# Performance work log

Measured on AMD Instinct MI355X. Metric: run time of the kernel, lower is better.

## Reference

```python
import jax, jax.numpy as jnp
import numpy as np

B, S, D, H, DFF = 2, 2048, 768, 12, 3072
DK = D // H
EPS = 1e-6
NEG = -1e9


def setup_inputs() -> dict:
    key = jax.random.key(0)
    ks = jax.random.split(key, 16)
    s = 1.0 / np.sqrt(D)
    inp = {
        'x': jax.random.normal(ks[0], (B, S, D), jnp.float32),
        'wq': jax.random.normal(ks[1], (D, D), jnp.float32) * s,
        'bq': jnp.zeros((D,), jnp.float32),
        'wk': jax.random.normal(ks[2], (D, D), jnp.float32) * s,
        'bk': jnp.zeros((D,), jnp.float32),
        'wv': jax.random.normal(ks[3], (D, D), jnp.float32) * s,
        'bv': jnp.zeros((D,), jnp.float32),
        'wo': jax.random.normal(ks[4], (D, D), jnp.float32) * s,
        'bo': jnp.zeros((D,), jnp.float32),
        'w1': jax.random.normal(ks[5], (D, DFF), jnp.float32) * s,
        'b1': jnp.zeros((DFF,), jnp.float32),
        'w2': jax.random.normal(ks[6], (DFF, D), jnp.float32) * (1.0 / np.sqrt(DFF)),
        'b2': jnp.zeros((D,), jnp.float32),
        'alpha1': jnp.ones((1,), jnp.float32),
        'beta1': jnp.zeros((1,), jnp.float32),
        'alpha2': jnp.ones((1,), jnp.float32),
        'beta2': jnp.zeros((1,), jnp.float32),
        'mask': jax.random.randint(ks[7], (1, 1, S, S), 0, 2, jnp.int32),
    }
    return inp


def layernorm(x, alpha, beta):
    # torch: mean and UNBIASED std (ddof=1), eps added to std (not variance)
    mean = jnp.mean(x, axis=-1, keepdims=True)
    std = jnp.std(x, axis=-1, keepdims=True, ddof=1)
    return alpha * (x - mean) / (std + EPS) + beta


def encoder_layer(x, wq, bq, wk, bk, wv, bv, wo, bo, w1, b1, w2, b2,
                  alpha1, beta1, alpha2, beta2, mask):
    # projections -> [B, H, S, DK]
    def split_heads(t):
        return t.reshape(B, S, H, DK).transpose(0, 2, 1, 3)
    q = split_heads(x @ wq + bq)
    k = split_heads(x @ wk + bk)
    v = split_heads(x @ wv + bv)
    scores = jnp.einsum('bhqd,bhkd->bhqk', q, k) / np.sqrt(DK)  # [B,H,S,S]
    scores = jnp.where(mask == 0, NEG, scores)
    attn = jax.nn.softmax(scores, axis=-1)
    ctx = jnp.einsum('bhqk,bhkd->bhqd', attn, v)
    ctx = ctx.transpose(0, 2, 1, 3).reshape(B, S, D)
    attn_out = ctx @ wo + bo
    x = layernorm(x + attn_out, alpha1, beta1)
    ff = jax.nn.relu(x @ w1 + b1) @ w2 + b2
    x = layernorm(x + ff, alpha2, beta2)
    return x


def reference(x, wq, bq, wk, bk, wv, bv, wo, bo, w1, b1, w2, b2,
              alpha1, beta1, alpha2, beta2, mask):
    return encoder_layer(x, wq, bq, wk, bk, wv, bv, wo, bo, w1, b1, w2, b2,
                         alpha1, beta1, alpha2, beta2, mask)
```

## Files before the change

### kernel.cpp

```cpp
#include <hip/hip_runtime.h>
#include <hip/hip_bf16.h>


typedef short short8 __attribute__((ext_vector_type(8)));
typedef float floatx4 __attribute__((ext_vector_type(4)));
typedef unsigned short ushort_t;
typedef ushort_t ushort4_t __attribute__((ext_vector_type(4)));

#define B_ 2
#define S_ 2048
#define D_ 768
#define H_ 12
#define DK_ 64
#define DFF_ 3072
#define M_ (B_ * S_)
#define RS_ (3 * D_)

#define LOG2E 1.44269504f
#define FMAX_SHIFT 16.0f

__device__ __forceinline__ float bf2f(ushort_t h) {
  union { unsigned int u; float f; } v; v.u = ((unsigned int)h) << 16; return v.f;
}
__device__ __forceinline__ ushort_t f2bf(float f) {
  union { float f; unsigned int u; } v; v.f = f;
  unsigned int u = v.u;
  unsigned int r = (u + 0x7fffu + ((u >> 16) & 1u)) >> 16;
  return (ushort_t)r;
}

__global__ __launch_bounds__(256) void prep_all(
    const float* __restrict__ wq, const float* __restrict__ wk,
    const float* __restrict__ wv, const float* __restrict__ wo,
    const float* __restrict__ w1, const float* __restrict__ w2,
    ushort_t* __restrict__ wTqkv, ushort_t* __restrict__ woT,
    ushort_t* __restrict__ w1T, ushort_t* __restrict__ w2T,
    const int* __restrict__ mask, ushort_t* __restrict__ maskp,
    const float* __restrict__ x, ushort_t* __restrict__ xb,
    const float* __restrict__ bq, const float* __restrict__ bk,
    const float* __restrict__ bv, float* __restrict__ bqkv) {
  __shared__ ushort_t t[32][33];
  const int blk = blockIdx.x, tid = threadIdx.x;
  if (blk < 6912) {
    const float* in; ushort_t* out; int K, N, bx, by;
    if (blk < 2304) {
      const int z = blk / 576, rr = blk % 576;
      in = (z == 0) ? wq : (z == 1) ? wk : (z == 2) ? wv : wo;
      out = (z < 3) ? (wTqkv + (size_t)z * D_ * D_) : woT;
      K = D_; N = D_; bx = rr % 24; by = rr / 24;
    } else if (blk < 4608) {
      const int rr = blk - 2304;
      in = w1; out = w1T; K = D_; N = DFF_; bx = rr % 96; by = rr / 96;
    } else {
      const int rr = blk - 4608;
      in = w2; out = w2T; K = DFF_; N = D_; bx = rr % 24; by = rr / 24;
    }
    const int nt = bx * 32, kt = by * 32;
    const int tx = tid & 31, ty = tid >> 5;
#pragma unroll
    for (int i = 0; i < 4; i++)
      t[ty + i * 8][tx] = f2bf(in[(size_t)(kt + ty + i * 8) * N + nt + tx]);
    __syncthreads();
#pragma unroll
    for (int i = 0; i < 4; i++)
      out[(size_t)(nt + ty + i * 8) * K + kt + tx] = t[tx][ty + i * 8];
  } else if (blk < 8960) {
    const int tt = (blk - 6912) * 256 + tid;
    const int q = tt >> 8;
    const int cc = tt & 255;
    const int k0 = (cc >> 3) * 64;
    const int g = cc & 7, f = g >> 2, lq = g & 3;
    const int* mrow = mask + (size_t)q * S_ + k0;
    const ushort_t cm = f2bf(-1.4427e9f);
    const ushort_t cu = f2bf(-FMAX_SHIFT * LOG2E);
    short8 o;
#pragma unroll
    for (int n2 = 0; n2 < 2; n2++)
#pragma unroll
      for (int r = 0; r < 4; r++) {
        const int kpl = 32 * f + 16 * n2 + 4 * lq + r;
        o[n2 * 4 + r] = (short)((mrow[kpl] == 0) ? cm : cu);
      }
    *(short8*)(maskp + (size_t)q * S_ + k0 + g * 8) = o;
  } else if (blk < 12032) {
    const int i = ((blk - 8960) * 256 + tid) * 4;
#pragma unroll
    for (int j = 0; j < 4; j++) xb[i + j] = f2bf(x[i + j]);
  } else {
    const int i = (blk - 12032) * 256 + tid;
    if (i < 3 * D_)
      bqkv[i] = (i < D_) ? bq[i] : (i < 2 * D_ ? bk[i - D_] : bv[i - 2 * D_]);
  }
}

template <int BN, int Z, bool VOUT>
__global__ __launch_bounds__(256) void gemm_bt_t(
    const ushort_t* __restrict__ A, const ushort_t* __restrict__ Bt,
    const float* __restrict__ bias, void* __restrict__ Cv,
    ushort_t* __restrict__ vtout,
    int M, int N, int K, int relu, int qcols, float qscale) {
  constexpr int WN = (BN == 128) ? 2 : 1;
  constexpr int WM = 4 / WN;
  constexpr int FI = 128 / WM / 16;
  constexpr int FJ = BN / WN / 16;
  constexpr bool SPLIT = (Z > 1);
  __shared__ __align__(16) ushort_t Al[2][128 * 32];
  __shared__ __align__(16) ushort_t Bl[2][BN * 32];
  const int tid = threadIdx.x;
  const int w = tid >> 6, lane = tid & 63;
  const int wm = (WN == 2) ? (w >> 1) : w;
  const int wn = (WN == 2) ? (w & 1) : 0;
  const int lq = lane >> 4, lr = lane & 15;

  const int NT_n = N / BN;
  const int mg = M >> 10;
  const int lin = blockIdx.x;
  const int xcd = lin & 7, idx = lin >> 3;
  const int m_t = xcd * mg + idx / (NT_n * Z);
  const int rem = idx % (NT_n * Z);
  const int n_t = rem % NT_n;
  const int z   = rem / NT_n;
  const int m0 = m_t * 128, n0 = n_t * BN;

  int kBeg = 0, kEnd = K;
  if (SPLIT) { const int part = K / Z; kBeg = z * part; kEnd = kBeg + part; }
  const int NT = (kEnd - kBeg) / 32;

  auto stage = [&](int kt, int s) {
    const int k0 = kBeg + kt * 32;
#pragma unroll
    for (int i = 0; i < 2; i++) {
      const int base = (w * 2 + i) * 512;
      const int e = base + lane * 8;
      const int row = e >> 5, col = e & 31;
      __builtin_amdgcn_global_load_lds(
          (const __attribute__((address_space(1))) void*)(A + (size_t)(m0 + row) * K + k0 + col),
          (__attribute__((address_space(3))) void*)(&Al[s][base]), 16, 0, 0);
    }
#pragma unroll
    for (int i = 0; i < BN / 64; i++) {
      const int base = (w * (BN / 64) + i) * 512;
      const int e = base + lane * 8;
      const int row = e >> 5, col = e & 31;
      __builtin_amdgcn_global_load_lds(
          (const __attribute__((address_space(1))) void*)(Bt + (size_t)(n0 + row) * K + k0 + col),
          (__attribute__((address_space(3))) void*)(&Bl[s][base]), 16, 0, 0);
    }
  };

  floatx4 acc[FI][FJ];
#pragma unroll
  for (int i = 0; i < FI; i++)
#pragma unroll
    for (int j = 0; j < FJ; j++) acc[i][j] = (floatx4){0.f, 0.f, 0.f, 0.f};

  stage(0, 0);
  for (int kt = 0; kt < NT; kt++) {
    const int s = kt & 1;
    __syncthreads();
    if (kt + 1 < NT) stage(kt + 1, s ^ 1);

    short8 af[FI], bf[FJ];
#pragma unroll
    for (int i = 0; i < FI; i++)
      af[i] = *(const short8*)&Al[s][(wm * (FI * 16) + i * 16 + lr) * 32 + lq * 8];
#pragma unroll
    for (int j = 0; j < FJ; j++)
      bf[j] = *(const short8*)&Bl[s][(wn * (FJ * 16) + j * 16 + lr) * 32 + lq * 8];
#pragma unroll
    for (int i = 0; i < FI; i++)
#pragma unroll
      for (int j = 0; j < FJ; j++)
        acc[i][j] = __builtin_amdgcn_mfma_f32_16x16x32_bf16(af[i], bf[j], acc[i][j], 0, 0, 0);
  }

#pragma unroll
  for (int i = 0; i < FI; i++) {
    const int m = m0 + wm * (FI * 16) + i * 16 + lq * 4;
#pragma unroll
    for (int j = 0; j < FJ; j++) {
      const int n = n0 + wn * (FJ * 16) + j * 16 + lr;
      if (SPLIT) {
        ushort_t* P = (ushort_t*)Cv + (size_t)z * M * N;
#pragma unroll
        for (int r = 0; r < 4; r++)
          P[(size_t)(m + r) * N + n] = f2bf(acc[i][j][r]);
      } else if (VOUT && n >= 2 * D_) {
        const int h = (n - 2 * D_) >> 6, d = (n - 2 * D_) & 63;
        const int bh = (m >> 11) * H_ + h;
        const int kp = m & (S_ - 1);
        const int kw = kp & 63;
        const int pos = (kp & ~63) + ((kw >> 5) << 5) + (((kw >> 2) & 3) << 3)
                      + (((kw >> 4) & 1) << 2);
        const float bv = bias[n];
        ushort4_t o;
#pragma unroll
        for (int r = 0; r < 4; r++) o[r] = f2bf(acc[i][j][r] + bv);
        *(ushort4_t*)(vtout + ((size_t)bh * DK_ + d) * S_ + pos) = o;
      } else {
        const float bv = bias[n];
#pragma unroll
        for (int r = 0; r < 4; r++) {
          float v = acc[i][j][r] + bv;
          if (n < qcols) v *= qscale;
          if (relu) v = v > 0.f ? v : 0.f;
          ((ushort_t*)Cv)[(size_t)(m + r) * N + n] = f2bf(v);
        }
      }
    }
  }
}

__global__ __launch_bounds__(256, 3) void flash_attn(
    const ushort_t* __restrict__ qkv, const ushort_t* __restrict__ vt,
    const ushort_t* __restrict__ maskp, ushort_t* __restrict__ ctx) {
  __shared__ __align__(16) ushort_t lds[2][2][64 * 64];
  const int tid = threadIdx.x;
  const int w = tid >> 6, lane = tid & 63;
  const int wq = w >> 1, wk = w & 1;
  const int lq = lane >> 4, lr = lane & 15;
  const int blk = blockIdx.x;
  const int bh = blk % (B_ * H_), qb = blk / (B_ * H_);
  const int b = bh / H_, h = bh % H_;
  const int q0 = qb * 64;
  const ushort_t* qbase = qkv + (size_t)(b * S_) * RS_ + h * DK_;
  const ushort_t* kbase = qbase + D_;
  const ushort_t* vtb   = vt + (size_t)bh * DK_ * S_;
  const ushort_t* mrow = maskp + (size_t)(q0 + wq * 32 + lr) * S_ + (4 * wk + lq) * 8;

  short8 qfr[2][2];
#pragma unroll
  for (int qf = 0; qf < 2; qf++)
#pragma unroll
    for (int f = 0; f < 2; f++)
      qfr[qf][f] = *(const short8*)(
          qbase + (size_t)(q0 + wq * 32 + qf * 16 + lr) * RS_ + f * 32 + lq * 8);

  auto stage = [&](int k0, int s) {
#pragma unroll
    for (int i = 0; i < 2; i++) {
      const int id = i * 256 + tid;
      const int row = id >> 3;
      const int cc = ((id & 7) ^ (row & 7)) * 8;
      const int dbase = (i * 256 + w * 64) * 8;
      __builtin_amdgcn_global_load_lds(
          (const __attribute__((address_space(1))) void*)(kbase + (size_t)(k0 + row) * RS_ + cc),
          (__attribute__((address_space(3))) void*)(&lds[s][0][dbase]), 16, 0, 0);
      __builtin_amdgcn_global_load_lds(
          (const __attribute__((address_space(1))) void*)(vtb + (size_t)row * S_ + k0 + cc),
          (__attribute__((address_space(3))) void*)(&lds[s][1][dbase]), 16, 0, 0);
    }
  };

  floatx4 oacc[2][4], oli[2];
#pragma unroll
  for (int qf = 0; qf < 2; qf++) {
    oli[qf] = (floatx4){0.f, 0.f, 0.f, 0.f};
#pragma unroll
    for (int dt = 0; dt < 4; dt++) oacc[qf][dt] = (floatx4){0.f, 0.f, 0.f, 0.f};
  }
  short8 ones;
#pragma unroll
  for (int j = 0; j < 8; j++) ones[j] = (short)0x3F80;

  short8 bb[2], bbn[2];
#pragma unroll
  for (int qf = 0; qf < 2; qf++)
    bb[qf] = *(const short8*)(mrow + (size_t)qf * 16 * S_);

  stage(0, 0);
  __syncthreads();

  const int sw8 = lr & 7;
  const int c0 = (lq ^ sw8) * 8;
  const int c1 = ((4 + lq) ^ sw8) * 8;
  const int cW = ((4 * wk + lq) ^ sw8) * 8;

  constexpr int NT = S_ / 64;
  for (int t = 0; t < NT; t++) {
    const int s = t & 1;
    if (t + 1 < NT) {
      stage((t + 1) * 64, s ^ 1);
#pragma unroll
      for (int qf = 0; qf < 2; qf++)
        bbn[qf] = *(const short8*)(mrow + (size_t)qf * 16 * S_ + (t + 1) * 64);
    }

    const ushort_t* kl = &lds[s][0][0];
    const ushort_t* vl = &lds[s][1][0];

    floatx4 sacc[2][2];
#pragma unroll
    for (int qf = 0; qf < 2; qf++)
#pragma unroll
      for (int n2 = 0; n2 < 2; n2++)
#pragma unroll
        for (int r = 0; r < 4; r++)
          sacc[qf][n2][r] = bf2f((ushort_t)bb[qf][n2 * 4 + r]);

#pragma unroll
    for (int n2 = 0; n2 < 2; n2++) {
      const int krow = ((2 * wk + n2) * 16 + lr) * 64;
      short8 a0 = *(const short8*)(kl + krow + c0);
      short8 a1 = *(const short8*)(kl + krow + c1);
#pragma unroll
      for (int qf = 0; qf < 2; qf++) {
        sacc[qf][n2] = __builtin_amdgcn_mfma_f32_16x16x32_bf16(a0, qfr[qf][0], sacc[qf][n2], 0, 0, 0);
        sacc[qf][n2] = __builtin_amdgcn_mfma_f32_16x16x32_bf16(a1, qfr[qf][1], sacc[qf][n2], 0, 0, 0);
      }
    }

    short8 pf[2];
#pragma unroll
    for (int qf = 0; qf < 2; qf++) {
      union { __hip_bfloat162 h2[4]; short8 v; } u;
#pragma unroll
      for (int jj = 0; jj < 4; jj++) {
        const int e0 = jj * 2, e1 = jj * 2 + 1;
        float2 p2;
        p2.x = __builtin_amdgcn_exp2f(sacc[qf][e0 >> 2][e0 & 3]);
        p2.y = __builtin_amdgcn_exp2f(sacc[qf][e1 >> 2][e1 & 3]);
        u.h2[jj] = __float22bfloat162_rn(p2);
      }
      pf[qf] = u.v;
    }

#pragma unroll
    for (int dt = 0; dt < 4; dt++) {
      const short8 vfr = *(const short8*)(vl + (dt * 16 + lr) * 64 + cW);
#pragma unroll
      for (int qf = 0; qf < 2; qf++)
        oacc[qf][dt] = __builtin_amdgcn_mfma_f32_16x16x32_bf16(vfr, pf[qf], oacc[qf][dt], 0, 0, 0);
    }
#pragma unroll
    for (int qf = 0; qf < 2; qf++)
      oli[qf] = __builtin_amdgcn_mfma_f32_16x16x32_bf16(ones, pf[qf], oli[qf], 0, 0, 0);

    if (t + 1 < NT) {
      bb[0] = bbn[0];
      bb[1] = bbn[1];
    }
    __syncthreads();
  }

  float* ex = (float*)&lds[0][0][0];
  if (wk == 1) {
    float* dst = ex + (size_t)(wq * 64 + lane) * 37;
#pragma unroll
    for (int qf = 0; qf < 2; qf++)
#pragma unroll
      for (int dt = 0; dt < 4; dt++)
#pragma unroll
        for (int r = 0; r < 4; r++)
          dst[qf * 16 + dt * 4 + r] = oacc[qf][dt][r];
    dst[32] = oli[0][0];
    dst[33] = oli[1][0];
  }
  __syncthreads();
  if (wk == 0) {
    const float* src = ex + (size_t)(wq * 64 + lane) * 37;
#pragma unroll
    for (int qf = 0; qf < 2; qf++)
#pragma unroll
      for (int dt = 0; dt < 4; dt++)
#pragma unroll
        for (int r = 0; r < 4; r++)
          oacc[qf][dt][r] += src[qf * 16 + dt * 4 + r];
    const float inv0 = 1.f / (oli[0][0] + src[32] + 1e-30f);
    const float inv1 = 1.f / (oli[1][0] + src[33] + 1e-30f);
#pragma unroll
    for (int qf = 0; qf < 2; qf++) {
      const float inv = qf ? inv1 : inv0;
      const size_t row = (size_t)(b * S_ + q0 + wq * 32 + qf * 16 + lr) * D_ + h * DK_;
#pragma unroll
      for (int dt = 0; dt < 4; dt++) {
        ushort4_t o;
#pragma unroll
        for (int r = 0; r < 4; r++) o[r] = f2bf(oacc[qf][dt][r] * inv);
        *(ushort4_t*)(ctx + row + dt * 16 + lq * 4) = o;
      }
    }
  }
}

template <int NP, bool XF, bool OF>
__global__ __launch_bounds__(256) void add_ln_comb(
    const void* __restrict__ xv, const ushort_t* __restrict__ P,
    const float* __restrict__ cb,
    const float* __restrict__ alpha, const float* __restrict__ beta,
    void* __restrict__ outv) {
  const int row = blockIdx.x, tid = threadIdx.x;
  const int w = tid >> 6, lane = tid & 63;
  __shared__ float red[8];
  float v[3];
#pragma unroll
  for (int i = 0; i < 3; i++) {
    const int c = tid + i * 256;
    const size_t idx = (size_t)row * D_ + c;
    float xv_;
    if (XF) xv_ = ((const float*)xv)[idx];
    else    xv_ = bf2f(((const ushort_t*)xv)[idx]);
    float ps = cb[c];
#pragma unroll
    for (int p = 0; p < NP; p++) ps += bf2f(P[idx + (size_t)p * M_ * D_]);
    v[i] = xv_ + ps;
  }
  float s = v[0] + v[1] + v[2];
#pragma unroll
  for (int off = 1; off < 64; off <<= 1) s += __shfl_xor(s, off);
  if (lane == 0) red[w] = s;
  __syncthreads();
  const float mean = (red[0] + red[1] + red[2] + red[3]) / (float)D_;
  float d = 0.f;
#pragma unroll
  for (int i = 0; i < 3; i++) { const float t = v[i] - mean; d += t * t; }
#pragma unroll
  for (int off = 1; off < 64; off <<= 1) d += __shfl_xor(d, off);
  if (lane == 0) red[4 + w] = d;
  __syncthreads();
  const float var = (red[4] + red[5] + red[6] + red[7]) / (float)(D_ - 1);
  const float inv = 1.f / (sqrtf(var) + 1e-6f);
  const float a = alpha[0] * inv, bt = beta[0];
#pragma unroll
  for (int i = 0; i < 3; i++) {
    const int c = tid + i * 256;
    const float o = a * (v[i] - mean) + bt;
    if (OF) ((float*)outv)[(size_t)row * D_ + c] = o;
    else    ((ushort_t*)outv)[(size_t)row * D_ + c] = f2bf(o);
  }
}

extern "C" void kernel_launch(void* const* d_in, const int* in_sizes, int n_in,
                              void* d_out, int out_size, void* d_ws, size_t ws_size,
                              hipStream_t stream) {
  const float* x   = (const float*)d_in[0];
  const float* wq  = (const float*)d_in[1];
  const float* bq  = (const float*)d_in[2];
  const float* wk  = (const float*)d_in[3];
  const float* bk  = (const float*)d_in[4];
  const float* wv  = (const float*)d_in[5];
  const float* bv  = (const float*)d_in[6];
  const float* wo  = (const float*)d_in[7];
  const float* bo  = (const float*)d_in[8];
  const float* w1  = (const float*)d_in[9];
  const float* b1  = (const float*)d_in[10];
  const float* w2  = (const float*)d_in[11];
  const float* b2  = (const float*)d_in[12];
  const float* a1  = (const float*)d_in[13];
  const float* be1 = (const float*)d_in[14];
  const float* a2  = (const float*)d_in[15];
  const float* be2 = (const float*)d_in[16];
  const int*   msk = (const int*)d_in[17];

  const size_t E_xb    = 0;
  const size_t E_wTqkv = E_xb    + (size_t)M_ * D_;
  const size_t E_woT   = E_wTqkv + (size_t)3 * D_ * D_;
  const size_t E_w1T   = E_woT   + (size_t)D_ * D_;
  const size_t E_w2T   = E_w1T   + (size_t)DFF_ * D_;
  const size_t E_bqkv  = E_w2T   + (size_t)D_ * DFF_;
  const size_t E_qkv   = E_bqkv  + (size_t)2 * 3 * D_;
  const size_t E_ctx   = E_qkv   + (size_t)M_ * 3 * D_;
  const size_t E_attn  = E_ctx   + (size_t)M_ * D_;
  const size_t E_x1    = E_attn  + (size_t)M_ * D_;
  const size_t E_h1    = E_x1    + (size_t)M_ * D_;
  const size_t E_ff    = E_h1    + (size_t)M_ * DFF_;
  const size_t E_total = E_ff    + (size_t)M_ * D_;
  if (ws_size < E_total * sizeof(ushort_t)) return;

  ushort_t* ws    = (ushort_t*)d_ws;
  ushort_t* xb    = ws + E_xb;
  ushort_t* wTqkv = ws + E_wTqkv;
  ushort_t* woT   = ws + E_woT;
  ushort_t* w1T   = ws + E_w1T;
  ushort_t* w2T   = ws + E_w2T;
  float*    bqkv  = (float*)(ws + E_bqkv);
  ushort_t* qkv   = ws + E_qkv;
  ushort_t* ctx   = ws + E_ctx;
  ushort_t* x1    = ws + E_x1;
  ushort_t* h1    = ws + E_h1;
  ushort_t* maskp = ws + E_h1;
  ushort_t* vt    = ws + E_h1 + (size_t)S_ * S_;
  ushort_t* Pattn = ws + E_h1;
  ushort_t* Pff2  = ws + E_qkv;

  const float SCALE_Q = 0.125f * LOG2E;

  prep_all<<<12041, 256, 0, stream>>>(wq, wk, wv, wo, w1, w2,
                                      wTqkv, woT, w1T, w2T,
                                      msk, maskp, x, xb, bq, bk, bv, bqkv);

  gemm_bt_t<64, 1, true><<<1152, 256, 0, stream>>>(
      xb, wTqkv, bqkv, qkv, vt, M_, 3 * D_, D_, 0, D_, SCALE_Q);
  flash_attn<<<(B_ * H_) * (S_ / 64), 256, 0, stream>>>(qkv, vt, maskp, ctx);
  gemm_bt_t<64, 4, false><<<1536, 256, 0, stream>>>(
      ctx, woT, nullptr, Pattn, nullptr, M_, D_, D_, 0, 0, 1.f);
  add_ln_comb<4, false, false><<<M_, 256, 0, stream>>>(
      xb, Pattn, bo, a1, be1, x1);
  gemm_bt_t<128, 1, false><<<768, 256, 0, stream>>>(
      x1, w1T, b1, h1, nullptr, M_, DFF_, D_, 1, 0, 1.f);
  gemm_bt_t<64, 4, false><<<1536, 256, 0, stream>>>(
      h1, w2T, nullptr, Pff2, nullptr, M_, D_, DFF_, 0, 0, 1.f);
  add_ln_comb<4, false, true><<<M_, 256, 0, stream>>>(
      x1, Pff2, b2, a2, be2, d_out);
}
```

Baseline: 303.9 us.

## Stage mask tiles through LDS, vectorize add-LayerNorm, halve split-K for out/FF2 GEMMs

The flash attention kernel now copies the 64x64 mask tile into a third LDS buffer with async global-to-LDS loads and reads the bias from LDS. The per-thread global mask prefetch registers are gone, at the cost of 50% more shared memory per block. The add+LayerNorm kernel uses 192 threads, each handling 4 contiguous elements with vector loads and stores. The output-projection and FF2 GEMMs go from 4-way to 2-way split-K, which halves the partial-sum traffic read by LayerNorm but leaves fewer blocks in flight.

```diff
diff --git a/kernel.cpp b/kernel.cpp
--- a/kernel.cpp
+++ b/kernel.cpp
@@ -214,7 +214,7 @@
 __global__ __launch_bounds__(256, 3) void flash_attn(
     const ushort_t* __restrict__ qkv, const ushort_t* __restrict__ vt,
     const ushort_t* __restrict__ maskp, ushort_t* __restrict__ ctx) {
-  __shared__ __align__(16) ushort_t lds[2][2][64 * 64];
+  __shared__ __align__(16) ushort_t lds[2][3][64 * 64];
   const int tid = threadIdx.x;
   const int w = tid >> 6, lane = tid & 63;
   const int wq = w >> 1, wk = w & 1;
@@ -226,7 +226,7 @@
   const ushort_t* qbase = qkv + (size_t)(b * S_) * RS_ + h * DK_;
   const ushort_t* kbase = qbase + D_;
   const ushort_t* vtb   = vt + (size_t)bh * DK_ * S_;
-  const ushort_t* mrow = maskp + (size_t)(q0 + wq * 32 + lr) * S_ + (4 * wk + lq) * 8;
+  const ushort_t* mb    = maskp + (size_t)q0 * S_;
 
   short8 qfr[2][2];
 #pragma unroll
@@ -249,6 +249,9 @@
       __builtin_amdgcn_global_load_lds(
           (const __attribute__((address_space(1))) void*)(vtb + (size_t)row * S_ + k0 + cc),
           (__attribute__((address_space(3))) void*)(&lds[s][1][dbase]), 16, 0, 0);
+      __builtin_amdgcn_global_load_lds(
+          (const __attribute__((address_space(1))) void*)(mb + (size_t)row * S_ + k0 + cc),
+          (__attribute__((address_space(3))) void*)(&lds[s][2][dbase]), 16, 0, 0);
     }
   };
 
@@ -262,11 +265,6 @@
   short8 ones;
 #pragma unroll
   for (int j = 0; j < 8; j++) ones[j] = (short)0x3F80;
-
-  short8 bb[2], bbn[2];
-#pragma unroll
-  for (int qf = 0; qf < 2; qf++)
-    bb[qf] = *(const short8*)(mrow + (size_t)qf * 16 * S_);
 
   stage(0, 0);
   __syncthreads();
@@ -279,24 +277,22 @@
   constexpr int NT = S_ / 64;
   for (int t = 0; t < NT; t++) {
     const int s = t & 1;
-    if (t + 1 < NT) {
-      stage((t + 1) * 64, s ^ 1);
-#pragma unroll
-      for (int qf = 0; qf < 2; qf++)
-        bbn[qf] = *(const short8*)(mrow + (size_t)qf * 16 * S_ + (t + 1) * 64);
-    }
+    if (t + 1 < NT) stage((t + 1) * 64, s ^ 1);
 
     const ushort_t* kl = &lds[s][0][0];
     const ushort_t* vl = &lds[s][1][0];
+    const ushort_t* ml = &lds[s][2][0];
 
     floatx4 sacc[2][2];
 #pragma unroll
-    for (int qf = 0; qf < 2; qf++)
+    for (int qf = 0; qf < 2; qf++) {
+      const short8 bb = *(const short8*)(ml + (wq * 32 + qf * 16 + lr) * 64 + cW);
 #pragma unroll
       for (int n2 = 0; n2 < 2; n2++)
 #pragma unroll
         for (int r = 0; r < 4; r++)
-          sacc[qf][n2][r] = bf2f((ushort_t)bb[qf][n2 * 4 + r]);
+          sacc[qf][n2][r] = bf2f((ushort_t)bb[n2 * 4 + r]);
+    }
 
 #pragma unroll
     for (int n2 = 0; n2 < 2; n2++) {
@@ -336,10 +332,6 @@
     for (int qf = 0; qf < 2; qf++)
       oli[qf] = __builtin_amdgcn_mfma_f32_16x16x32_bf16(ones, pf[qf], oli[qf], 0, 0, 0);
 
-    if (t + 1 < NT) {
-      bb[0] = bbn[0];
-      bb[1] = bbn[1];
-    }
     __syncthreads();
   }
 
@@ -384,49 +376,63 @@
 }
 
 template <int NP, bool XF, bool OF>
-__global__ __launch_bounds__(256) void add_ln_comb(
+__global__ __launch_bounds__(192) void add_ln_comb(
     const void* __restrict__ xv, const ushort_t* __restrict__ P,
     const float* __restrict__ cb,
     const float* __restrict__ alpha, const float* __restrict__ beta,
     void* __restrict__ outv) {
   const int row = blockIdx.x, tid = threadIdx.x;
   const int w = tid >> 6, lane = tid & 63;
-  __shared__ float red[8];
-  float v[3];
-#pragma unroll
-  for (int i = 0; i < 3; i++) {
-    const int c = tid + i * 256;
-    const size_t idx = (size_t)row * D_ + c;
-    float xv_;
-    if (XF) xv_ = ((const float*)xv)[idx];
-    else    xv_ = bf2f(((const ushort_t*)xv)[idx]);
-    float ps = cb[c];
-#pragma unroll
-    for (int p = 0; p < NP; p++) ps += bf2f(P[idx + (size_t)p * M_ * D_]);
-    v[i] = xv_ + ps;
-  }
-  float s = v[0] + v[1] + v[2];
+  __shared__ float red[6];
+  const size_t base = (size_t)row * D_ + tid * 4;
+  float v[4];
+  {
+    float xv4[4];
+    if (XF) {
+      const float4 xx = *(const float4*)((const float*)xv + base);
+      xv4[0] = xx.x; xv4[1] = xx.y; xv4[2] = xx.z; xv4[3] = xx.w;
+    } else {
+      const ushort4_t xx = *(const ushort4_t*)((const ushort_t*)xv + base);
+#pragma unroll
+      for (int r = 0; r < 4; r++) xv4[r] = bf2f(xx[r]);
+    }
+    const float4 cb4 = *(const float4*)(cb + tid * 4);
+    float ps[4] = {cb4.x, cb4.y, cb4.z, cb4.w};
+#pragma unroll
+    for (int p = 0; p < NP; p++) {
+      const ushort4_t pp = *(const ushort4_t*)(P + base + (size_t)p * M_ * D_);
+#pragma unroll
+      for (int r = 0; r < 4; r++) ps[r] += bf2f(pp[r]);
+    }
+#pragma unroll
+    for (int r = 0; r < 4; r++) v[r] = xv4[r] + ps[r];
+  }
+  float s = (v[0] + v[1]) + (v[2] + v[3]);
 #pragma unroll
   for (int off = 1; off < 64; off <<= 1) s += __shfl_xor(s, off);
   if (lane == 0) red[w] = s;
   __syncthreads();
-  const float mean = (red[0] + red[1] + red[2] + red[3]) / (float)D_;
+  const float mean = (red[0] + red[1] + red[2]) / (float)D_;
   float d = 0.f;
 #pragma unroll
-  for (int i = 0; i < 3; i++) { const float t = v[i] - mean; d += t * t; }
+  for (int r = 0; r < 4; r++) { const float t = v[r] - mean; d += t * t; }
 #pragma unroll
   for (int off = 1; off < 64; off <<= 1) d += __shfl_xor(d, off);
-  if (lane == 0) red[4 + w] = d;
+  if (lane == 0) red[3 + w] = d;
   __syncthreads();
-  const float var = (red[4] + red[5] + red[6] + red[7]) / (float)(D_ - 1);
+  const float var = (red[3] + red[4] + red[5]) / (float)(D_ - 1);
   const float inv = 1.f / (sqrtf(var) + 1e-6f);
   const float a = alpha[0] * inv, bt = beta[0];
-#pragma unroll
-  for (int i = 0; i < 3; i++) {
-    const int c = tid + i * 256;
-    const float o = a * (v[i] - mean) + bt;
-    if (OF) ((float*)outv)[(size_t)row * D_ + c] = o;
-    else    ((ushort_t*)outv)[(size_t)row * D_ + c] = f2bf(o);
+  if (OF) {
+    float4 o;
+    o.x = a * (v[0] - mean) + bt;  o.y = a * (v[1] - mean) + bt;
+    o.z = a * (v[2] - mean) + bt;  o.w = a * (v[3] - mean) + bt;
+    *(float4*)((float*)outv + base) = o;
+  } else {
+    ushort4_t o;
+#pragma unroll
+    for (int r = 0; r < 4; r++) o[r] = f2bf(a * (v[r] - mean) + bt);
+    *(ushort4_t*)((ushort_t*)outv + base) = o;
   }
 }
 
@@ -492,14 +498,14 @@
   gemm_bt_t<64, 1, true><<<1152, 256, 0, stream>>>(
       xb, wTqkv, bqkv, qkv, vt, M_, 3 * D_, D_, 0, D_, SCALE_Q);
   flash_attn<<<(B_ * H_) * (S_ / 64), 256, 0, stream>>>(qkv, vt, maskp, ctx);
-  gemm_bt_t<64, 4, false><<<1536, 256, 0, stream>>>(
+  gemm_bt_t<64, 2, false><<<768, 256, 0, stream>>>(
       ctx, woT, nullptr, Pattn, nullptr, M_, D_, D_, 0, 0, 1.f);
-  add_ln_comb<4, false, false><<<M_, 256, 0, stream>>>(
+  add_ln_comb<2, false, false><<<M_, 192, 0, stream>>>(
       xb, Pattn, bo, a1, be1, x1);
   gemm_bt_t<128, 1, false><<<768, 256, 0, stream>>>(
       x1, w1T, b1, h1, nullptr, M_, DFF_, D_, 1, 0, 1.f);
-  gemm_bt_t<64, 4, false><<<1536, 256, 0, stream>>>(
+  gemm_bt_t<64, 2, false><<<768, 256, 0, stream>>>(
       h1, w2T, nullptr, Pff2, nullptr, M_, D_, DFF_, 0, 0, 1.f);
-  add_ln_comb<4, false, true><<<M_, 256, 0, stream>>>(
+  add_ln_comb<2, false, true><<<M_, 192, 0, stream>>>(
       x1, Pff2, b2, a2, be2, d_out);
 }
```

Measured after the change: 288.4 us. -5.1%, faster.
